# Optimization experiments

Hardware: AMD Instinct MI355X
Metric: run time of the kernel (lower is better)

The kernel has to match this reference:

```python
import jax, jax.numpy as jnp
import numpy as np

H, D = 4, 32
EMB = H * D  # 128
COUNTS = [30000, 20000, 25000, 50000]  # pesticide, disease, plant, event
EDGE_TYPES = [(0, 1), (1, 0), (2, 1), (1, 2), (3, 0), (0, 3), (3, 2), (2, 3)]
E = 200000
INV_SQRT_D = 1.0 / float(np.sqrt(D))


def layer_norm(x, g, b, eps=1e-5):
    m = x.mean(-1, keepdims=True)
    v = ((x - m) ** 2).mean(-1, keepdims=True)
    return (x - m) * jax.lax.rsqrt(v + eps) * g + b


def hgt_block(xs, edges, kqvW, kqvb, outW, outb, skip, a_rel, m_rel, p_rel, ln_g, ln_b):
    # type-specific K/Q/V projections -> [N, H, D]
    K, Q, V = [], [], []
    for t in range(4):
        kqv = jnp.einsum('nc,kdc->knd', xs[t], kqvW[t]) + kqvb[t][:, None, :]
        K.append(kqv[0].reshape(-1, H, D))
        Q.append(kqv[1].reshape(-1, H, D))
        V.append(kqv[2].reshape(-1, H, D))
    per_dst = {t: [] for t in range(4)}
    for r, (s, t) in enumerate(EDGE_TYPES):
        src, dst = edges[r, 0], edges[r, 1]
        k_rel = jnp.einsum('ehd,hdf->ehf', K[s][src], a_rel[r])  # relation-specific key transform
        v_rel = jnp.einsum('ehd,hdf->ehf', V[s][src], m_rel[r])  # relation-specific message transform
        logit = (k_rel * Q[t][dst]).sum(-1) * p_rel[r] * INV_SQRT_D  # [E, H]
        per_dst[t].append((logit, v_rel, dst))
    outs = []
    for t in range(4):
        N = xs[t].shape[0]
        logits = jnp.concatenate([p[0] for p in per_dst[t]], axis=0)
        vals = jnp.concatenate([p[1] for p in per_dst[t]], axis=0)
        idx = jnp.concatenate([p[2] for p in per_dst[t]], axis=0)
        # single segment softmax per destination node across ALL incoming edge types (PyG HGTConv)
        mx = jax.ops.segment_max(logits, idx, num_segments=N)
        ex = jnp.exp(logits - mx[idx])
        den = jax.ops.segment_sum(ex, idx, num_segments=N)
        alpha = ex / jnp.maximum(den[idx], 1e-16)
        agg = jax.ops.segment_sum(vals * alpha[..., None], idx, num_segments=N).reshape(N, EMB)
        o = jax.nn.gelu(agg, approximate=False) @ outW[t].T + outb[t]
        sg = jax.nn.sigmoid(skip[t])
        o = sg * o + (1.0 - sg) * xs[t]  # HGTConv learnable skip
        # HGTBlock: residual add, LayerNorm, ReLU (dropout = identity in eval)
        outs.append(jax.nn.relu(layer_norm(o + xs[t], ln_g, ln_b)))
    return outs


def fusion(seq, inW, inb, outW, outb, g, b):
    # seq: [N, 3, EMB]; torch MultiheadAttention self-attention, then mean + LN
    qkv = seq @ inW.T + inb  # [N, 3, 3*EMB]
    q, k, v = jnp.split(qkv, 3, axis=-1)
    heads = lambda x: x.reshape(x.shape[0], 3, H, D).transpose(0, 2, 1, 3)  # [N,H,3,D]
    q, k, v = heads(q), heads(k), heads(v)
    att = jax.nn.softmax(jnp.einsum('nhqd,nhkd->nhqk', q, k) * INV_SQRT_D, axis=-1)
    o = jnp.einsum('nhqk,nhkd->nhqd', att, v).transpose(0, 2, 1, 3).reshape(-1, 3, EMB)
    o = o @ outW.T + outb
    return layer_norm(o.mean(axis=1), g, b)


def _forward(x_pest, x_dis, x_plant, edges, proj_W, proj_b, event_emb, kqv_W, kqv_b,
             out_W, out_b, skip, a_rel, m_rel, p_rel, blk_ln_g, blk_ln_b,
             fin_W, fin_b, fout_W, fout_b, f_ln_g, f_ln_b):
    xs = [jax.nn.relu(x_pest @ proj_W[0].T + proj_b[0]),
          jax.nn.relu(x_dis @ proj_W[1].T + proj_b[1]),
          jax.nn.relu(x_plant @ proj_W[2].T + proj_b[2]),
          event_emb]  # event_emb(arange(N)) == the full table
    layers = []
    cur = xs
    for l in range(3):
        cur = hgt_block(cur, edges, kqv_W[l], kqv_b[l], out_W[l], out_b[l], skip[l],
                        a_rel[l], m_rel[l], p_rel[l], blk_ln_g[l], blk_ln_b[l])
        layers.append(cur)
    outs = []
    for j, t in enumerate([0, 1, 2]):  # pesticide, disease, plant
        seq = jnp.stack([layers[0][t], layers[1][t], layers[2][t]], axis=1)
        outs.append(fusion(seq, fin_W[j], fin_b[j], fout_W[j], fout_b[j], f_ln_g[j], f_ln_b[j]))
    return jnp.concatenate(outs, axis=0)  # [30000+20000+25000, 128]


def setup_inputs() -> dict:
    key = jax.random.key(0)
    ks = iter(jax.random.split(key, 64))
    nrm = lambda shape, s=0.05: jax.random.normal(next(ks), shape, dtype=jnp.float32) * s
    rows = []
    for s, t in EDGE_TYPES:
        rows.append(jnp.stack([jax.random.randint(next(ks), (E,), 0, COUNTS[s]),
                               jax.random.randint(next(ks), (E,), 0, COUNTS[t])]))
    return {
        'x_pest': nrm((COUNTS[0], 64), 1.0),
        'x_dis': nrm((COUNTS[1], 64), 1.0),
        'x_plant': nrm((COUNTS[2], 64), 1.0),
        'edges': jnp.stack(rows).astype(jnp.int32),  # [8, 2, E]
        'proj_W': nrm((3, EMB, 64)), 'proj_b': nrm((3, EMB)),
        'event_emb': nrm((COUNTS[3], EMB), 1.0),
        'kqv_W': nrm((3, 4, 3, EMB, EMB)), 'kqv_b': nrm((3, 4, 3, EMB)),
        'out_W': nrm((3, 4, EMB, EMB)), 'out_b': nrm((3, 4, EMB)),
        'skip': nrm((3, 4), 1.0),
        'a_rel': nrm((3, 8, H, D, D), 0.1), 'm_rel': nrm((3, 8, H, D, D), 0.1),
        'p_rel': jnp.ones((3, 8, H), jnp.float32),
        'blk_ln_g': jnp.ones((3, EMB), jnp.float32), 'blk_ln_b': jnp.zeros((3, EMB), jnp.float32),
        'fin_W': nrm((3, 3 * EMB, EMB)), 'fin_b': nrm((3, 3 * EMB)),
        'fout_W': nrm((3, EMB, EMB)), 'fout_b': nrm((3, EMB)),
        'f_ln_g': jnp.ones((3, EMB), jnp.float32), 'f_ln_b': jnp.zeros((3, EMB), jnp.float32),
    }


def reference(x_pest, x_dis, x_plant, edges, proj_W, proj_b, event_emb, kqv_W, kqv_b,
              out_W, out_b, skip, a_rel, m_rel, p_rel, blk_ln_g, blk_ln_b,
              fin_W, fin_b, fout_W, fout_b, f_ln_g, f_ln_b):
    return _forward(x_pest, x_dis, x_plant, edges, proj_W, proj_b, event_emb, kqv_W, kqv_b,
                    out_W, out_b, skip, a_rel, m_rel, p_rel, blk_ln_g, blk_ln_b,
                    fin_W, fin_b, fout_W, fout_b, f_ln_g, f_ln_b)
```

## Files before the change

kernel.cpp:

```cpp
#include <hip/hip_runtime.h>
#include <math.h>

#define E_CNT 200000
typedef unsigned short bfu;
typedef unsigned short u16;
typedef __attribute__((ext_vector_type(8))) short bh8;
typedef __attribute__((ext_vector_type(4))) float f4;

__device__ __forceinline__ float gelu_f(float x) {
    return 0.5f * x * (1.0f + erff(x * 0.70710678118654752f));
}
__device__ __forceinline__ float bf2f(bfu u) { return __uint_as_float(((unsigned)u) << 16); }
__device__ __forceinline__ bfu f2bf(float f) {
    unsigned u = __float_as_uint(f);
    unsigned r = u + 0x7FFFu + ((u >> 16) & 1u);
    return (bfu)(r >> 16);
}
__device__ __forceinline__ int rsrc_of(int r) {
    const int a[8] = {0, 1, 2, 1, 3, 0, 3, 2}; return a[r];
}
__device__ __forceinline__ int rdst_of(int r) {
    const int a[8] = {1, 0, 1, 2, 0, 3, 2, 3}; return a[r];
}
__device__ __forceinline__ int rpoff_of(int r) {
    const int a[9] = {0, 20001, 50002, 70003, 95004, 125005, 175006, 200007, 250008};
    return a[r];
}

__global__ __launch_bounds__(256) void fill_val(float* p, int n, float v) {
    int i = blockIdx.x * 256 + threadIdx.x;
    if (i < n) p[i] = v;
}

__global__ __launch_bounds__(256) void cvt_pack(
    const float* __restrict__ out_W, const float* __restrict__ kqv_W,
    const float* __restrict__ fin_W, const float* __restrict__ fout_W,
    const float* __restrict__ event_emb, const float* __restrict__ proj_W,
    bfu* __restrict__ OWB, bfu* __restrict__ KWB, bfu* __restrict__ FINWB,
    bfu* __restrict__ FOUTWB, bfu* __restrict__ EVB, bfu* __restrict__ PJWB)
{
    int i = blockIdx.x * 256 + threadIdx.x;
    const float* src; bfu* dst; size_t so, dox;
    if (i < 49152) { src = out_W; dst = OWB; so = (size_t)i * 4; dox = so; }
    else if (i < 98304) {
        int j = i - 49152; int m = j >> 12; int o = (j & 4095) * 4;
        src = kqv_W; dst = KWB;
        so = (size_t)m * 3 * 16384 + o; dox = (size_t)m * 16384 + o;
    }
    else if (i < 135168) { int j = i - 98304; src = fin_W; dst = FINWB; so = (size_t)j * 4; dox = so; }
    else if (i < 147456) { int j = i - 135168; src = fout_W; dst = FOUTWB; so = (size_t)j * 4; dox = so; }
    else if (i < 1747456) { int j = i - 147456; src = event_emb; dst = EVB; so = (size_t)j * 4; dox = so; }
    else if (i < 1753600) { int j = i - 1747456; src = proj_W; dst = PJWB; so = (size_t)j * 4; dox = so; }
    else return;
    float4 v = *(const float4*)(src + so);
    uint2 u;
    u.x = ((unsigned)f2bf(v.x)) | (((unsigned)f2bf(v.y)) << 16);
    u.y = ((unsigned)f2bf(v.z)) | (((unsigned)f2bf(v.w)) << 16);
    *(uint2*)(dst + dox) = u;
}

__global__ __launch_bounds__(256) void hist_all(const int* __restrict__ edges, int* __restrict__ rp) {
    int i = blockIdx.x * 256 + threadIdx.x;
    if (i >= 8 * E_CNT) return;
    int r = i / E_CNT, e = i - r * E_CNT;
    int d = edges[(size_t)(2 * r + 1) * E_CNT + e];
    atomicAdd(&rp[rpoff_of(r) + d + 1], 1);
}
__global__ __launch_bounds__(1024) void scan_part(int* __restrict__ a, int* __restrict__ part, int n) {
    __shared__ int lds[1024];
    int t = threadIdx.x, i = blockIdx.x * 1024 + t;
    int v = (i < n) ? a[i] : 0;
    lds[t] = v;
    __syncthreads();
    for (int off = 1; off < 1024; off <<= 1) {
        int u = (t >= off) ? lds[t - off] : 0;
        __syncthreads();
        lds[t] += u;
        __syncthreads();
    }
    if (i < n) a[i] = lds[t];
    if (t == 1023) part[blockIdx.x] = lds[1023];
}
__global__ __launch_bounds__(256) void scan_tot(int* __restrict__ part, int nb) {
    __shared__ int lds[256];
    int t = threadIdx.x;
    int v = (t < nb) ? part[t] : 0;
    lds[t] = v;
    __syncthreads();
    for (int off = 1; off < 256; off <<= 1) {
        int u = (t >= off) ? lds[t - off] : 0;
        __syncthreads();
        lds[t] += u;
        __syncthreads();
    }
    if (t < nb) part[t] = lds[t];
}
__global__ __launch_bounds__(1024) void scan_add(int* __restrict__ a, const int* __restrict__ part, int n) {
    int b = blockIdx.x + 1;
    int i = b * 1024 + threadIdx.x;
    if (i < n) a[i] += part[b - 1];
}
__global__ __launch_bounds__(256) void scatter_all(
    const int* __restrict__ edges, const int* __restrict__ RP,
    int* __restrict__ cur, u16* __restrict__ SIDX) {
    int i = blockIdx.x * 256 + threadIdx.x;
    if (i >= 8 * E_CNT) return;
    int r = i / E_CNT, e = i - r * E_CNT;
    int d = edges[(size_t)(2 * r + 1) * E_CNT + e];
    int pos = RP[rpoff_of(r) + d] + atomicAdd(&cur[r * 50000 + d], 1);
    SIDX[pos] = (u16)edges[(size_t)(2 * r) * E_CNT + e];
}

struct PDesc { const float* X; const bfu* W; const float* bias; bfu* Y; int N; int bend; };
struct PBatch { PDesc d[3]; };

__global__ __launch_bounds__(256) void mgemm_proj(PBatch pb) {
    int b = blockIdx.x;
    int gi = 0;
    #pragma unroll
    for (int k = 0; k < 2; ++k) gi += (b >= pb.d[k].bend) ? 1 : 0;
    const float* X = pb.d[0].X; const bfu* W = pb.d[0].W;
    const float* bi = pb.d[0].bias; bfu* Y = pb.d[0].Y;
    int N = pb.d[0].N, bstart = 0;
    #pragma unroll
    for (int k = 1; k < 3; ++k) {
        if (gi == k) {
            X = pb.d[k].X; W = pb.d[k].W; bi = pb.d[k].bias; Y = pb.d[k].Y;
            N = pb.d[k].N; bstart = pb.d[k - 1].bend;
        }
    }
    int bloc = b - bstart;
    const int tid = threadIdx.x;
    const int wave = tid >> 6, lane = tid & 63;
    const int row16 = lane & 15, kgrp = lane >> 4;
    const int r_base = bloc * 128 + wave * 32;
    f4 acc[2][8];
    #pragma unroll
    for (int t = 0; t < 2; ++t)
        #pragma unroll
        for (int n = 0; n < 8; ++n) acc[t][n] = (f4){0.f, 0.f, 0.f, 0.f};
    bh8 az = {0, 0, 0, 0, 0, 0, 0, 0};
    #pragma unroll
    for (int kb = 0; kb < 2; ++kb) {
        bh8 a[2] = {az, az};
        #pragma unroll
        for (int t = 0; t < 2; ++t) {
            int ar = r_base + t * 16 + row16;
            if (ar < N) {
                const float* xp = X + (size_t)ar * 64 + kb * 32 + kgrp * 8;
                float4 xa = *(const float4*)xp;
                float4 xb = *(const float4*)(xp + 4);
                a[t][0] = (short)f2bf(xa.x); a[t][1] = (short)f2bf(xa.y);
                a[t][2] = (short)f2bf(xa.z); a[t][3] = (short)f2bf(xa.w);
                a[t][4] = (short)f2bf(xb.x); a[t][5] = (short)f2bf(xb.y);
                a[t][6] = (short)f2bf(xb.z); a[t][7] = (short)f2bf(xb.w);
            }
        }
        #pragma unroll
        for (int n = 0; n < 8; ++n) {
            bh8 bv = *(const bh8*)(W + (size_t)(n * 16 + row16) * 64 + kb * 32 + kgrp * 8);
            acc[0][n] = __builtin_amdgcn_mfma_f32_16x16x32_bf16(a[0], bv, acc[0][n], 0, 0, 0);
            acc[1][n] = __builtin_amdgcn_mfma_f32_16x16x32_bf16(a[1], bv, acc[1][n], 0, 0, 0);
        }
    }
    #pragma unroll
    for (int t = 0; t < 2; ++t) {
        const int crow0 = r_base + t * 16 + kgrp * 4;
        #pragma unroll
        for (int n = 0; n < 8; ++n) {
            int col = n * 16 + row16;
            float bn = bi[col];
            #pragma unroll
            for (int j = 0; j < 4; ++j) {
                int row = crow0 + j;
                if (row < N) Y[(size_t)row * 128 + col] = f2bf(fmaxf(acc[t][n][j] + bn, 0.f));
            }
        }
    }
}

__global__ __launch_bounds__(256) void build_rel(
    const float* __restrict__ kqvW_l, const float* __restrict__ kqvb_l,
    const float* __restrict__ a_l, const float* __restrict__ m_l,
    bfu* __restrict__ WQAB, float* __restrict__ BQA,
    bfu* __restrict__ WVMB, float* __restrict__ BVM)
{
    __shared__ float As[32][33];
    __shared__ float Ws[32][129];
    int tid = threadIdx.x;
    int b = blockIdx.x;
    if (b < 32) {
        int r = b >> 2, h = b & 3;
        int dt = rdst_of(r);
        const float* Wq = kqvW_l + ((size_t)dt * 3 + 1) * 16384;
        const float* bq = kqvb_l + ((size_t)dt * 3 + 1) * 128;
        const float* A = a_l + (size_t)r * 4096 + h * 1024;
        for (int v = tid; v < 1024; v += 256) As[v >> 5][v & 31] = A[v];
        for (int v = tid; v < 4096; v += 256)
            Ws[v >> 7][v & 127] = Wq[(size_t)(h * 32 + (v >> 7)) * 128 + (v & 127)];
        __syncthreads();
        int c = tid & 127, half = tid >> 7;
        for (int d = half; d < 32; d += 2) {
            float acc = 0.f;
            #pragma unroll
            for (int f = 0; f < 32; ++f) acc = fmaf(As[d][f], Ws[f][c], acc);
            WQAB[((size_t)r * 128 + h * 32 + d) * 128 + c] = f2bf(acc);
        }
        if (tid < 32) {
            int d = tid;
            float acc = 0.f;
            #pragma unroll
            for (int f = 0; f < 32; ++f) acc = fmaf(As[d][f], bq[h * 32 + f], acc);
            BQA[(size_t)r * 128 + h * 32 + d] = acc;
        }
    } else {
        int bb2 = b - 32;
        int r = bb2 >> 2, h = bb2 & 3;
        int st = rsrc_of(r);
        const float* Wv = kqvW_l + ((size_t)st * 3 + 2) * 16384;
        const float* bv = kqvb_l + ((size_t)st * 3 + 2) * 128;
        const float* M = m_l + (size_t)r * 4096 + h * 1024;
        for (int v = tid; v < 1024; v += 256) As[v >> 5][v & 31] = M[v];
        for (int v = tid; v < 4096; v += 256)
            Ws[v >> 7][v & 127] = Wv[(size_t)(h * 32 + (v >> 7)) * 128 + (v & 127)];
        __syncthreads();
        int c = tid & 127, half = tid >> 7;
        for (int f = half; f < 32; f += 2) {
            float acc = 0.f;
            #pragma unroll
            for (int d = 0; d < 32; ++d) acc = fmaf(As[d][f], Ws[d][c], acc);
            WVMB[((size_t)r * 128 + h * 32 + f) * 128 + c] = f2bf(acc);
        }
        if (tid < 32) {
            int f = tid;
            float acc = 0.f;
            #pragma unroll
            for (int d = 0; d < 32; ++d) acc = fmaf(As[d][f], bv[h * 32 + d], acc);
            BVM[(size_t)r * 128 + h * 32 + f] = acc;
        }
    }
}

struct GDesc { const bfu* X; const bfu* W; const float* bias; bfu* Y; int N; int ldy; int bend; };
struct GBatch { GDesc d[9]; };

__global__ __launch_bounds__(256) void mgemm_batch(GBatch gb) {
    int b = blockIdx.x;
    int gi = 0;
    #pragma unroll
    for (int k = 0; k < 8; ++k) gi += (b >= gb.d[k].bend) ? 1 : 0;
    const bfu* X = gb.d[0].X; const bfu* W = gb.d[0].W;
    const float* bi = gb.d[0].bias; bfu* Y = gb.d[0].Y;
    int N = gb.d[0].N, ldy = gb.d[0].ldy, bstart = 0;
    #pragma unroll
    for (int k = 1; k < 9; ++k) {
        if (gi == k) {
            X = gb.d[k].X; W = gb.d[k].W; bi = gb.d[k].bias; Y = gb.d[k].Y;
            N = gb.d[k].N; ldy = gb.d[k].ldy; bstart = gb.d[k - 1].bend;
        }
    }
    int bloc = b - bstart;
    const int tid = threadIdx.x;
    const int wave = tid >> 6, lane = tid & 63;
    const int row16 = lane & 15, kgrp = lane >> 4;
    const int r_base = bloc * 128 + wave * 32;
    f4 acc[2][8];
    #pragma unroll
    for (int t = 0; t < 2; ++t)
        #pragma unroll
        for (int n = 0; n < 8; ++n) acc[t][n] = (f4){0.f, 0.f, 0.f, 0.f};
    bh8 az = {0, 0, 0, 0, 0, 0, 0, 0};
    #pragma unroll
    for (int kb = 0; kb < 4; ++kb) {
        int ar0 = r_base + row16, ar1 = r_base + 16 + row16;
        bh8 a0 = az, a1 = az;
        if (ar0 < N) a0 = *(const bh8*)(X + (size_t)ar0 * 128 + kb * 32 + kgrp * 8);
        if (ar1 < N) a1 = *(const bh8*)(X + (size_t)ar1 * 128 + kb * 32 + kgrp * 8);
        #pragma unroll
        for (int n = 0; n < 8; ++n) {
            bh8 bv = *(const bh8*)(W + (size_t)(n * 16 + row16) * 128 + kb * 32 + kgrp * 8);
            acc[0][n] = __builtin_amdgcn_mfma_f32_16x16x32_bf16(a0, bv, acc[0][n], 0, 0, 0);
            acc[1][n] = __builtin_amdgcn_mfma_f32_16x16x32_bf16(a1, bv, acc[1][n], 0, 0, 0);
        }
    }
    #pragma unroll
    for (int t = 0; t < 2; ++t) {
        const int crow0 = r_base + t * 16 + kgrp * 4;
        #pragma unroll
        for (int n = 0; n < 8; ++n) {
            int col = n * 16 + row16;
            float bn = bi[col];
            #pragma unroll
            for (int j = 0; j < 4; ++j) {
                int row = crow0 + j;
                if (row < N) Y[(size_t)row * ldy + col] = f2bf(acc[t][n][j] + bn);
            }
        }
    }
}

__global__ __launch_bounds__(256) void agg_dual(
    const bfu* QAA, const bfu* __restrict__ QAB,
    const bfu* __restrict__ KA, const bfu* __restrict__ VMA,
    const bfu* __restrict__ KB, const bfu* __restrict__ VMB,
    const int* __restrict__ rpA, const int* __restrict__ rpB,
    const u16* __restrict__ sidx,
    const float* __restrict__ prlA, const float* __restrict__ prlB,
    bfu* ACC, int Nn)
{
    int n = blockIdx.x * 4 + (threadIdx.x >> 6);
    if (n >= Nn) return;
    int l = threadIdx.x & 63;
    int h = l >> 4;
    const float scl = 0.17677669529663687f;

    float m = -3.0e38f, d = 0.f, a0 = 0.f, a1 = 0.f;

    auto upd = [&](float s, unsigned vu) {
        float nm = fmaxf(m, s);
        float sc = __expf(m - nm), w = __expf(s - nm);
        d = d * sc + w;
        a0 = fmaf(w, bf2f((bfu)vu), a0 * sc);
        a1 = fmaf(w, bf2f((bfu)(vu >> 16)), a1 * sc);
        m = nm;
    };

    auto rel = [&](const bfu* QA, const bfu* __restrict__ K, const bfu* __restrict__ VM,
                   const int* __restrict__ rp, const float* __restrict__ prl) {
        unsigned qu = *(const unsigned*)(QA + (size_t)n * 128 + 2 * l);
        float q0 = bf2f((bfu)qu), q1 = bf2f((bfu)(qu >> 16));
        float ph = prl[h] * scl;
        int i = rp[n], e1 = rp[n + 1];
        for (; i + 3 < e1; i += 4) {
            int sa = sidx[i], sb = sidx[i + 1], sc2 = sidx[i + 2], sd = sidx[i + 3];
            unsigned ka = *(const unsigned*)(K + (size_t)sa * 128 + 2 * l);
            unsigned kb = *(const unsigned*)(K + (size_t)sb * 128 + 2 * l);
            unsigned kc = *(const unsigned*)(K + (size_t)sc2 * 128 + 2 * l);
            unsigned kd = *(const unsigned*)(K + (size_t)sd * 128 + 2 * l);
            unsigned va = *(const unsigned*)(VM + (size_t)sa * 128 + 2 * l);
            unsigned vb = *(const unsigned*)(VM + (size_t)sb * 128 + 2 * l);
            unsigned vc = *(const unsigned*)(VM + (size_t)sc2 * 128 + 2 * l);
            unsigned vd = *(const unsigned*)(VM + (size_t)sd * 128 + 2 * l);
            float s0 = fmaf(bf2f((bfu)ka), q0, bf2f((bfu)(ka >> 16)) * q1);
            float s1 = fmaf(bf2f((bfu)kb), q0, bf2f((bfu)(kb >> 16)) * q1);
            float s2 = fmaf(bf2f((bfu)kc), q0, bf2f((bfu)(kc >> 16)) * q1);
            float s3 = fmaf(bf2f((bfu)kd), q0, bf2f((bfu)(kd >> 16)) * q1);
            #pragma unroll
            for (int off = 1; off <= 8; off <<= 1) {
                s0 += __shfl_xor(s0, off);
                s1 += __shfl_xor(s1, off);
                s2 += __shfl_xor(s2, off);
                s3 += __shfl_xor(s3, off);
            }
            upd(s0 * ph, va);
            upd(s1 * ph, vb);
            upd(s2 * ph, vc);
            upd(s3 * ph, vd);
        }
        for (; i < e1; ++i) {
            int sa = sidx[i];
            unsigned ka = *(const unsigned*)(K + (size_t)sa * 128 + 2 * l);
            unsigned va = *(const unsigned*)(VM + (size_t)sa * 128 + 2 * l);
            float s0 = fmaf(bf2f((bfu)ka), q0, bf2f((bfu)(ka >> 16)) * q1);
            #pragma unroll
            for (int off = 1; off <= 8; off <<= 1) s0 += __shfl_xor(s0, off);
            upd(s0 * ph, va);
        }
    };
    rel(QAA, KA, VMA, rpA, prlA);
    rel(QAB, KB, VMB, rpB, prlB);

    float rd = 1.f / fmaxf(d, 1e-16f);
    float y0 = gelu_f(a0 * rd);
    float y1 = gelu_f(a1 * rd);
    unsigned ou = ((unsigned)f2bf(y0)) | (((unsigned)f2bf(y1)) << 16);
    *(unsigned*)(ACC + (size_t)n * 128 + 2 * l) = ou;
}

__global__ __launch_bounds__(256) void mgemm_epi_layer(
    const bfu* __restrict__ A, const bfu* __restrict__ W, const float* __restrict__ bias,
    const bfu* __restrict__ Xr, const float* __restrict__ skp,
    const float* __restrict__ g, const float* __restrict__ bb,
    bfu* __restrict__ Y, int N)
{
    const int tid = threadIdx.x;
    const int wave = tid >> 6, lane = tid & 63;
    const int row16 = lane & 15, kgrp = lane >> 4;
    const int r_base = blockIdx.x * 64 + wave * 16;
    const int arow = r_base + row16;
    f4 acc[8];
    #pragma unroll
    for (int n = 0; n < 8; ++n) acc[n] = (f4){0.f, 0.f, 0.f, 0.f};
    bh8 az = {0, 0, 0, 0, 0, 0, 0, 0};
    #pragma unroll
    for (int kb = 0; kb < 4; ++kb) {
        bh8 a = az;
        if (arow < N) a = *(const bh8*)(A + (size_t)arow * 128 + kb * 32 + kgrp * 8);
        #pragma unroll
        for (int n = 0; n < 8; ++n) {
            bh8 bv = *(const bh8*)(W + (size_t)(n * 16 + row16) * 128 + kb * 32 + kgrp * 8);
            acc[n] = __builtin_amdgcn_mfma_f32_16x16x32_bf16(a, bv, acc[n], 0, 0, 0);
        }
    }
    const int crow0 = r_base + kgrp * 4;
    float sg = 1.f / (1.f + expf(-skp[0]));
    float z[8][4];
    #pragma unroll
    for (int n = 0; n < 8; ++n) {
        float bn = bias[n * 16 + row16];
        #pragma unroll
        for (int j = 0; j < 4; ++j) z[n][j] = acc[n][j] + bn;
    }
    #pragma unroll
    for (int j = 0; j < 4; ++j) {
        int row = crow0 + j;
        if (row >= N) continue;
        #pragma unroll
        for (int n = 0; n < 8; ++n) {
            float xr = bf2f(Xr[(size_t)row * 128 + n * 16 + row16]);
            z[n][j] = sg * z[n][j] + (1.f - sg) * xr + xr;
        }
    }
    float s[4], q[4];
    #pragma unroll
    for (int j = 0; j < 4; ++j) {
        s[j] = 0.f; q[j] = 0.f;
        #pragma unroll
        for (int n = 0; n < 8; ++n) { s[j] += z[n][j]; q[j] += z[n][j] * z[n][j]; }
    }
    #pragma unroll
    for (int off = 1; off <= 8; off <<= 1) {
        #pragma unroll
        for (int j = 0; j < 4; ++j) {
            s[j] += __shfl_xor(s[j], off);
            q[j] += __shfl_xor(q[j], off);
        }
    }
    #pragma unroll
    for (int j = 0; j < 4; ++j) {
        int row = crow0 + j;
        if (row >= N) continue;
        float mean = s[j] * (1.f / 128.f);
        float var = q[j] * (1.f / 128.f) - mean * mean;
        float inv = rsqrtf(var + 1e-5f);
        #pragma unroll
        for (int n = 0; n < 8; ++n) {
            int col = n * 16 + row16;
            float y = (z[n][j] - mean) * inv * g[col] + bb[col];
            Y[(size_t)row * 128 + col] = f2bf(fmaxf(y, 0.f));
        }
    }
}

__global__ __launch_bounds__(256) void mgemm_epi_ln(
    const bfu* __restrict__ X, const bfu* __restrict__ W, const float* __restrict__ bias,
    const float* __restrict__ g, const float* __restrict__ bb,
    float* __restrict__ Y, int N)
{
    const int tid = threadIdx.x;
    const int wave = tid >> 6, lane = tid & 63;
    const int row16 = lane & 15, kgrp = lane >> 4;
    const int r_base = blockIdx.x * 64 + wave * 16;
    const int arow = r_base + row16;
    f4 acc[8];
    #pragma unroll
    for (int n = 0; n < 8; ++n) acc[n] = (f4){0.f, 0.f, 0.f, 0.f};
    bh8 az = {0, 0, 0, 0, 0, 0, 0, 0};
    #pragma unroll
    for (int kb = 0; kb < 4; ++kb) {
        bh8 a = az;
        if (arow < N) a = *(const bh8*)(X + (size_t)arow * 128 + kb * 32 + kgrp * 8);
        #pragma unroll
        for (int n = 0; n < 8; ++n) {
            bh8 bv = *(const bh8*)(W + (size_t)(n * 16 + row16) * 128 + kb * 32 + kgrp * 8);
            acc[n] = __builtin_amdgcn_mfma_f32_16x16x32_bf16(a, bv, acc[n], 0, 0, 0);
        }
    }
    const int crow0 = r_base + kgrp * 4;
    float z[8][4];
    #pragma unroll
    for (int n = 0; n < 8; ++n) {
        float bn = bias[n * 16 + row16];
        #pragma unroll
        for (int j = 0; j < 4; ++j) z[n][j] = acc[n][j] + bn;
    }
    float s[4], q[4];
    #pragma unroll
    for (int j = 0; j < 4; ++j) {
        s[j] = 0.f; q[j] = 0.f;
        #pragma unroll
        for (int n = 0; n < 8; ++n) { s[j] += z[n][j]; q[j] += z[n][j] * z[n][j]; }
    }
    #pragma unroll
    for (int off = 1; off <= 8; off <<= 1) {
        #pragma unroll
        for (int j = 0; j < 4; ++j) {
            s[j] += __shfl_xor(s[j], off);
            q[j] += __shfl_xor(q[j], off);
        }
    }
    #pragma unroll
    for (int j = 0; j < 4; ++j) {
        int row = crow0 + j;
        if (row >= N) continue;
        float mean = s[j] * (1.f / 128.f);
        float var = q[j] * (1.f / 128.f) - mean * mean;
        float inv = rsqrtf(var + 1e-5f);
        #pragma unroll
        for (int n = 0; n < 8; ++n) {
            int col = n * 16 + row16;
            Y[(size_t)row * 128 + col] = (z[n][j] - mean) * inv * g[col] + bb[col];
        }
    }
}

__global__ __launch_bounds__(256) void attn_fuse(
    const bfu* __restrict__ QKV, bfu* __restrict__ OM, int M)
{
    int n = blockIdx.x * 4 + (threadIdx.x >> 6);
    int l = threadIdx.x & 63;
    if (n >= M) return;
    const bfu* base = QKV + (size_t)n * 1152;
    float q[3][2], k[3][2], v[3][2];
    #pragma unroll
    for (int p = 0; p < 3; ++p) {
        q[p][0] = bf2f(base[(0 * 3 + p) * 128 + l]);
        q[p][1] = bf2f(base[(0 * 3 + p) * 128 + l + 64]);
        k[p][0] = bf2f(base[(1 * 3 + p) * 128 + l]);
        k[p][1] = bf2f(base[(1 * 3 + p) * 128 + l + 64]);
        v[p][0] = bf2f(base[(2 * 3 + p) * 128 + l]);
        v[p][1] = bf2f(base[(2 * 3 + p) * 128 + l + 64]);
    }
    float lgA[3][3], lgB[3][3];
    #pragma unroll
    for (int qi = 0; qi < 3; ++qi)
        #pragma unroll
        for (int ki = 0; ki < 3; ++ki) {
            float s0 = q[qi][0] * k[ki][0];
            float s1 = q[qi][1] * k[ki][1];
            #pragma unroll
            for (int off = 1; off <= 16; off <<= 1) {
                s0 += __shfl_xor(s0, off);
                s1 += __shfl_xor(s1, off);
            }
            lgA[qi][ki] = s0 * 0.17677669529663687f;
            lgB[qi][ki] = s1 * 0.17677669529663687f;
        }
    float oA = 0.f, oB = 0.f;
    #pragma unroll
    for (int qi = 0; qi < 3; ++qi) {
        float mA = fmaxf(lgA[qi][0], fmaxf(lgA[qi][1], lgA[qi][2]));
        float e0 = __expf(lgA[qi][0] - mA), e1 = __expf(lgA[qi][1] - mA), e2 = __expf(lgA[qi][2] - mA);
        float rd = 1.f / (e0 + e1 + e2);
        oA += (e0 * v[0][0] + e1 * v[1][0] + e2 * v[2][0]) * rd;
        float mB = fmaxf(lgB[qi][0], fmaxf(lgB[qi][1], lgB[qi][2]));
        float f0 = __expf(lgB[qi][0] - mB), f1 = __expf(lgB[qi][1] - mB), f2 = __expf(lgB[qi][2] - mB);
        float rdB = 1.f / (f0 + f1 + f2);
        oB += (f0 * v[0][1] + f1 * v[1][1] + f2 * v[2][1]) * rdB;
    }
    OM[(size_t)n * 128 + l] = f2bf(oA * (1.f / 3.f));
    OM[(size_t)n * 128 + l + 64] = f2bf(oB * (1.f / 3.f));
}

extern "C" void kernel_launch(void* const* d_in, const int* in_sizes, int n_in,
                              void* d_out, int out_size, void* d_ws, size_t ws_size,
                              hipStream_t stream)
{
    const float* x_pest   = (const float*)d_in[0];
    const float* x_dis    = (const float*)d_in[1];
    const float* x_plant  = (const float*)d_in[2];
    const int*   edges    = (const int*)d_in[3];
    const float* proj_W   = (const float*)d_in[4];
    const float* proj_b   = (const float*)d_in[5];
    const float* event_emb= (const float*)d_in[6];
    const float* kqv_W    = (const float*)d_in[7];
    const float* kqv_b    = (const float*)d_in[8];
    const float* out_W    = (const float*)d_in[9];
    const float* out_b    = (const float*)d_in[10];
    const float* skip     = (const float*)d_in[11];
    const float* a_rel    = (const float*)d_in[12];
    const float* m_rel    = (const float*)d_in[13];
    const float* p_rel    = (const float*)d_in[14];
    const float* blk_ln_g = (const float*)d_in[15];
    const float* blk_ln_b = (const float*)d_in[16];
    const float* fin_W    = (const float*)d_in[17];
    const float* fin_b    = (const float*)d_in[18];
    const float* fout_W   = (const float*)d_in[19];
    const float* fout_b   = (const float*)d_in[20];
    const float* f_ln_g   = (const float*)d_in[21];
    const float* f_ln_b   = (const float*)d_in[22];
    float* out = (float*)d_out;

    static const int NT[4]  = {30000, 20000, 25000, 50000};
    static const int OFF[4] = {0, 30000, 50000, 75000};
    static const int RPOFF[9] = {0, 20001, 50002, 70003, 95004, 125005, 175006, 200007, 250008};
    static const int DG[4][2][2] = { {{1,1},{4,3}}, {{0,0},{2,2}}, {{3,1},{6,3}}, {{5,0},{7,2}} };

    char* wsb = (char*)d_ws;
    size_t ob = 0;
    auto alc = [&](size_t bytes) -> void* {
        void* p = wsb + ob; ob += (bytes + 255) & ~(size_t)255; return p;
    };
    bfu* LK0  = (bfu*)alc((size_t)75000 * 128 * 2);
    bfu* LK1  = (bfu*)alc((size_t)75000 * 128 * 2);
    bfu* POOL = (bfu*)alc((size_t)210000 * 128 * 2);
    bfu* WQAB = (bfu*)alc((size_t)8 * 16384 * 2);
    float* BQA = (float*)alc((size_t)8 * 128 * 4);
    bfu* WVMB = (bfu*)alc((size_t)8 * 16384 * 2);
    float* BVM = (float*)alc((size_t)8 * 128 * 4);
    bfu* KWB  = (bfu*)alc((size_t)12 * 16384 * 2);
    bfu* OWB  = (bfu*)alc((size_t)12 * 16384 * 2);
    bfu* FINWB = (bfu*)alc((size_t)3 * 49152 * 2);
    bfu* FOUTWB = (bfu*)alc((size_t)3 * 16384 * 2);
    bfu* PJWB = (bfu*)alc((size_t)3 * 8192 * 2);
    int* RP   = (int*)alc((size_t)250008 * 4);
    int* PART = (int*)alc(1024);
    u16* SIDX = (u16*)alc((size_t)8 * E_CNT * 2);
    if (ws_size < ob) {
        fill_val<<<(out_size + 255) / 256, 256, 0, stream>>>(out, out_size, 1e30f);
        return;
    }
    int* CUR = (int*)POOL;
    bfu* QKVf = POOL;
    bfu* OMB  = POOL + (size_t)20000 * 1152;

    bfu* EVB = (bfu*)out;
    bfu* XB  = (bfu*)((char*)out + 12800000);
    bfu* L2F = (bfu*)((char*)out + 19200000);

    cvt_pack<<<(1753600 + 255) / 256, 256, 0, stream>>>(
        out_W, kqv_W, fin_W, fout_W, event_emb, proj_W,
        OWB, KWB, FINWB, FOUTWB, EVB, PJWB);

    hipMemsetAsync(RP, 0, (size_t)250008 * 4, stream);
    const int eg8 = (8 * E_CNT + 255) / 256;
    hist_all<<<eg8, 256, 0, stream>>>(edges, RP);
    scan_part<<<245, 1024, 0, stream>>>(RP, PART, 250008);
    scan_tot<<<1, 256, 0, stream>>>(PART, 245);
    scan_add<<<244, 1024, 0, stream>>>(RP, PART, 250008);
    hipMemsetAsync(CUR, 0, (size_t)8 * 50000 * 4, stream);
    scatter_all<<<eg8, 256, 0, stream>>>(edges, RP, CUR, SIDX);

    {
        PBatch pb;
        const float* xin0[3] = {x_pest, x_dis, x_plant};
        int acc = 0;
        for (int t = 0; t < 3; ++t) {
            pb.d[t].X = xin0[t];
            pb.d[t].W = PJWB + (size_t)t * 8192;
            pb.d[t].bias = proj_b + (size_t)t * 128;
            pb.d[t].Y = XB + (size_t)OFF[t] * 128;
            pb.d[t].N = NT[t];
            acc += (NT[t] + 127) / 128;
            pb.d[t].bend = acc;
        }
        mgemm_proj<<<acc, 256, 0, stream>>>(pb);
    }

    auto launch_batch = [&](GDesc* ds, int cnt) {
        GBatch gb;
        int acc = 0;
        for (int i = 0; i < cnt; ++i) {
            gb.d[i] = ds[i];
            acc += (ds[i].N + 127) / 128;
            gb.d[i].bend = acc;
        }
        for (int i = cnt; i < 9; ++i) { gb.d[i] = gb.d[cnt - 1]; gb.d[i].bend = acc; }
        mgemm_batch<<<acc, 256, 0, stream>>>(gb);
    };

    for (int l = 0; l < 3; ++l) {
        const float* kqvW_l = kqv_W + (size_t)l * 12 * 16384;
        const float* kqvb_l = kqv_b + (size_t)l * 12 * 128;
        build_rel<<<64, 256, 0, stream>>>(kqvW_l, kqvb_l,
            a_rel + (size_t)l * 8 * 4096, m_rel + (size_t)l * 8 * 4096,
            WQAB, BQA, WVMB, BVM);

        auto feat_ptr = [&](int tt) -> const bfu* {
            if (tt == 3) return EVB;
            if (l == 0) return XB + (size_t)OFF[tt] * 128;
            return (l == 1 ? LK0 : LK1) + (size_t)OFF[tt] * 128;
        };

        int nord = (l == 2) ? 3 : 4;
        for (int dt = 0; dt < nord; ++dt) {
            int Ndt = NT[dt];
            int rA = DG[dt][0][0], sA = DG[dt][0][1];
            int rB = DG[dt][1][0], sB = DG[dt][1][1];
            int NsA = NT[sA], NsB = NT[sB];
            bfu* QA_A = POOL;
            bfu* QA_B = QA_A + (size_t)Ndt * 128;
            bfu* K_A  = QA_B + (size_t)Ndt * 128;
            bfu* VM_A = K_A + (size_t)NsA * 128;
            bfu* K_B  = VM_A + (size_t)NsA * 128;
            bfu* VM_B = K_B + (size_t)NsB * 128;

            GDesc ds[6];
            ds[0] = { feat_ptr(dt), WQAB + (size_t)rA * 16384, BQA + (size_t)rA * 128, QA_A, Ndt, 128, 0 };
            ds[1] = { feat_ptr(dt), WQAB + (size_t)rB * 16384, BQA + (size_t)rB * 128, QA_B, Ndt, 128, 0 };
            ds[2] = { feat_ptr(sA), KWB + (size_t)(l * 4 + sA) * 16384,
                      kqvb_l + ((size_t)sA * 3 + 0) * 128, K_A, NsA, 128, 0 };
            ds[3] = { feat_ptr(sA), WVMB + (size_t)rA * 16384, BVM + (size_t)rA * 128, VM_A, NsA, 128, 0 };
            ds[4] = { feat_ptr(sB), KWB + (size_t)(l * 4 + sB) * 16384,
                      kqvb_l + ((size_t)sB * 3 + 0) * 128, K_B, NsB, 128, 0 };
            ds[5] = { feat_ptr(sB), WVMB + (size_t)rB * 16384, BVM + (size_t)rB * 128, VM_B, NsB, 128, 0 };
            launch_batch(ds, 6);

            agg_dual<<<(Ndt + 3) / 4, 256, 0, stream>>>(
                QA_A, QA_B, K_A, VM_A, K_B, VM_B,
                RP + RPOFF[rA], RP + RPOFF[rB], SIDX,
                p_rel + (size_t)(l * 8 + rA) * 4, p_rel + (size_t)(l * 8 + rB) * 4,
                QA_A , Ndt);

            size_t wi = (size_t)l * 4 + dt;
            const bfu* xr = feat_ptr(dt);
            bfu* ydst = (dt == 3) ? EVB :
                        (l == 0 ? LK0 : (l == 1 ? LK1 : L2F)) + (size_t)OFF[dt] * 128;
            mgemm_epi_layer<<<(Ndt + 63) / 64, 256, 0, stream>>>(
                QA_A, OWB + wi * 16384, out_b + wi * 128, xr, skip + wi,
                blk_ln_g + (size_t)l * 128, blk_ln_b + (size_t)l * 128, ydst, Ndt);
        }
    }

    const int CH = 20000;
    for (int j = 0; j < 3; ++j) {
        int Nj = NT[j];
        for (int b0 = 0; b0 < Nj; b0 += CH) {
            int M = min(CH, Nj - b0);
            const bfu* srcs[3] = {
                LK0 + (size_t)(OFF[j] + b0) * 128,
                LK1 + (size_t)(OFF[j] + b0) * 128,
                L2F + (size_t)(OFF[j] + b0) * 128 };
            GDesc ds[9];
            int di = 0;
            for (int kk = 0; kk < 3; ++kk)
                for (int p = 0; p < 3; ++p) {
                    ds[di++] = { srcs[p], FINWB + (size_t)j * 49152 + (size_t)kk * 16384,
                                 fin_b + (size_t)j * 384 + kk * 128,
                                 QKVf + (size_t)(kk * 3 + p) * 128, M, 1152, 0 };
                }
            launch_batch(ds, 9);
            attn_fuse<<<(M + 3) / 4, 256, 0, stream>>>(QKVf, OMB, M);
            mgemm_epi_ln<<<(M + 63) / 64, 256, 0, stream>>>(
                OMB, FOUTWB + (size_t)j * 16384, fout_b + (size_t)j * 128,
                f_ln_g + (size_t)j * 128, f_ln_b + (size_t)j * 128,
                out + (size_t)(OFF[j] + b0) * 128, M);
        }
    }
}
```

Baseline: 1.702 ms.

## Interleave K and V rows and split online softmax into two chains

The projection GEMMs now write K and the relation-transformed V into one interleaved buffer with a 256-element row stride, so each gathered source node's K and V sit in the same 512-byte span. This is meant to improve locality of the random gathers in the aggregation kernel. The online-softmax state is split into two independent accumulators that alternate across unrolled edges and are merged at the end. That shortens the serial dependency chain of exp/fma updates, at the cost of extra registers and a final merge step.

```diff
diff --git a/kernel.cpp b/kernel.cpp
--- a/kernel.cpp
+++ b/kernel.cpp
@@ -301,8 +301,7 @@
 
 __global__ __launch_bounds__(256) void agg_dual(
     const bfu* QAA, const bfu* __restrict__ QAB,
-    const bfu* __restrict__ KA, const bfu* __restrict__ VMA,
-    const bfu* __restrict__ KB, const bfu* __restrict__ VMB,
+    const bfu* __restrict__ KVA, const bfu* __restrict__ KVB,
     const int* __restrict__ rpA, const int* __restrict__ rpB,
     const u16* __restrict__ sidx,
     const float* __restrict__ prlA, const float* __restrict__ prlB,
@@ -314,18 +313,27 @@
     int h = l >> 4;
     const float scl = 0.17677669529663687f;
 
-    float m = -3.0e38f, d = 0.f, a0 = 0.f, a1 = 0.f;
-
-    auto upd = [&](float s, unsigned vu) {
-        float nm = fmaxf(m, s);
-        float sc = __expf(m - nm), w = __expf(s - nm);
-        d = d * sc + w;
-        a0 = fmaf(w, bf2f((bfu)vu), a0 * sc);
-        a1 = fmaf(w, bf2f((bfu)(vu >> 16)), a1 * sc);
-        m = nm;
+    float m0 = -3.0e38f, d0 = 0.f, x0 = 0.f, y0 = 0.f;
+    float m1 = -3.0e38f, d1 = 0.f, x1 = 0.f, y1 = 0.f;
+
+    auto upd0 = [&](float s, unsigned vu) {
+        float nm = fmaxf(m0, s);
+        float sc = __expf(m0 - nm), w = __expf(s - nm);
+        d0 = d0 * sc + w;
+        x0 = fmaf(w, bf2f((bfu)vu), x0 * sc);
+        y0 = fmaf(w, bf2f((bfu)(vu >> 16)), y0 * sc);
+        m0 = nm;
     };
-
-    auto rel = [&](const bfu* QA, const bfu* __restrict__ K, const bfu* __restrict__ VM,
+    auto upd1 = [&](float s, unsigned vu) {
+        float nm = fmaxf(m1, s);
+        float sc = __expf(m1 - nm), w = __expf(s - nm);
+        d1 = d1 * sc + w;
+        x1 = fmaf(w, bf2f((bfu)vu), x1 * sc);
+        y1 = fmaf(w, bf2f((bfu)(vu >> 16)), y1 * sc);
+        m1 = nm;
+    };
+
+    auto rel = [&](const bfu* QA, const bfu* __restrict__ KV,
                    const int* __restrict__ rp, const float* __restrict__ prl) {
         unsigned qu = *(const unsigned*)(QA + (size_t)n * 128 + 2 * l);
         float q0 = bf2f((bfu)qu), q1 = bf2f((bfu)(qu >> 16));
@@ -333,14 +341,18 @@
         int i = rp[n], e1 = rp[n + 1];
         for (; i + 3 < e1; i += 4) {
             int sa = sidx[i], sb = sidx[i + 1], sc2 = sidx[i + 2], sd = sidx[i + 3];
-            unsigned ka = *(const unsigned*)(K + (size_t)sa * 128 + 2 * l);
-            unsigned kb = *(const unsigned*)(K + (size_t)sb * 128 + 2 * l);
-            unsigned kc = *(const unsigned*)(K + (size_t)sc2 * 128 + 2 * l);
-            unsigned kd = *(const unsigned*)(K + (size_t)sd * 128 + 2 * l);
-            unsigned va = *(const unsigned*)(VM + (size_t)sa * 128 + 2 * l);
-            unsigned vb = *(const unsigned*)(VM + (size_t)sb * 128 + 2 * l);
-            unsigned vc = *(const unsigned*)(VM + (size_t)sc2 * 128 + 2 * l);
-            unsigned vd = *(const unsigned*)(VM + (size_t)sd * 128 + 2 * l);
+            const bfu* pa = KV + (size_t)sa * 256 + 2 * l;
+            const bfu* pb = KV + (size_t)sb * 256 + 2 * l;
+            const bfu* pc = KV + (size_t)sc2 * 256 + 2 * l;
+            const bfu* pd = KV + (size_t)sd * 256 + 2 * l;
+            unsigned ka = *(const unsigned*)pa;
+            unsigned kb = *(const unsigned*)pb;
+            unsigned kc = *(const unsigned*)pc;
+            unsigned kd = *(const unsigned*)pd;
+            unsigned va = *(const unsigned*)(pa + 128);
+            unsigned vb = *(const unsigned*)(pb + 128);
+            unsigned vc = *(const unsigned*)(pc + 128);
+            unsigned vd = *(const unsigned*)(pd + 128);
             float s0 = fmaf(bf2f((bfu)ka), q0, bf2f((bfu)(ka >> 16)) * q1);
             float s1 = fmaf(bf2f((bfu)kb), q0, bf2f((bfu)(kb >> 16)) * q1);
             float s2 = fmaf(bf2f((bfu)kc), q0, bf2f((bfu)(kc >> 16)) * q1);
@@ -352,28 +364,35 @@
                 s2 += __shfl_xor(s2, off);
                 s3 += __shfl_xor(s3, off);
             }
-            upd(s0 * ph, va);
-            upd(s1 * ph, vb);
-            upd(s2 * ph, vc);
-            upd(s3 * ph, vd);
+            upd0(s0 * ph, va);
+            upd1(s1 * ph, vb);
+            upd0(s2 * ph, vc);
+            upd1(s3 * ph, vd);
         }
         for (; i < e1; ++i) {
             int sa = sidx[i];
-            unsigned ka = *(const unsigned*)(K + (size_t)sa * 128 + 2 * l);
-            unsigned va = *(const unsigned*)(VM + (size_t)sa * 128 + 2 * l);
+            const bfu* pa = KV + (size_t)sa * 256 + 2 * l;
+            unsigned ka = *(const unsigned*)pa;
+            unsigned va = *(const unsigned*)(pa + 128);
             float s0 = fmaf(bf2f((bfu)ka), q0, bf2f((bfu)(ka >> 16)) * q1);
             #pragma unroll
             for (int off = 1; off <= 8; off <<= 1) s0 += __shfl_xor(s0, off);
-            upd(s0 * ph, va);
+            upd0(s0 * ph, va);
         }
     };
-    rel(QAA, KA, VMA, rpA, prlA);
-    rel(QAB, KB, VMB, rpB, prlB);
+    rel(QAA, KVA, rpA, prlA);
+    rel(QAB, KVB, rpB, prlB);
+
+    float nm = fmaxf(m0, m1);
+    float sA = __expf(m0 - nm), sB = __expf(m1 - nm);
+    float d = d0 * sA + d1 * sB;
+    float a0 = x0 * sA + x1 * sB;
+    float a1 = y0 * sA + y1 * sB;
 
     float rd = 1.f / fmaxf(d, 1e-16f);
-    float y0 = gelu_f(a0 * rd);
-    float y1 = gelu_f(a1 * rd);
-    unsigned ou = ((unsigned)f2bf(y0)) | (((unsigned)f2bf(y1)) << 16);
+    float o0 = gelu_f(a0 * rd);
+    float o1 = gelu_f(a1 * rd);
+    unsigned ou = ((unsigned)f2bf(o0)) | (((unsigned)f2bf(o1)) << 16);
     *(unsigned*)(ACC + (size_t)n * 128 + 2 * l) = ou;
 }
 
@@ -690,24 +709,22 @@
             int NsA = NT[sA], NsB = NT[sB];
             bfu* QA_A = POOL;
             bfu* QA_B = QA_A + (size_t)Ndt * 128;
-            bfu* K_A  = QA_B + (size_t)Ndt * 128;
-            bfu* VM_A = K_A + (size_t)NsA * 128;
-            bfu* K_B  = VM_A + (size_t)NsA * 128;
-            bfu* VM_B = K_B + (size_t)NsB * 128;
+            bfu* KV_A = QA_B + (size_t)Ndt * 128;
+            bfu* KV_B = KV_A + (size_t)NsA * 256;
 
             GDesc ds[6];
             ds[0] = { feat_ptr(dt), WQAB + (size_t)rA * 16384, BQA + (size_t)rA * 128, QA_A, Ndt, 128, 0 };
             ds[1] = { feat_ptr(dt), WQAB + (size_t)rB * 16384, BQA + (size_t)rB * 128, QA_B, Ndt, 128, 0 };
             ds[2] = { feat_ptr(sA), KWB + (size_t)(l * 4 + sA) * 16384,
-                      kqvb_l + ((size_t)sA * 3 + 0) * 128, K_A, NsA, 128, 0 };
-            ds[3] = { feat_ptr(sA), WVMB + (size_t)rA * 16384, BVM + (size_t)rA * 128, VM_A, NsA, 128, 0 };
+                      kqvb_l + ((size_t)sA * 3 + 0) * 128, KV_A, NsA, 256, 0 };
+            ds[3] = { feat_ptr(sA), WVMB + (size_t)rA * 16384, BVM + (size_t)rA * 128, KV_A + 128, NsA, 256, 0 };
             ds[4] = { feat_ptr(sB), KWB + (size_t)(l * 4 + sB) * 16384,
-                      kqvb_l + ((size_t)sB * 3 + 0) * 128, K_B, NsB, 128, 0 };
-            ds[5] = { feat_ptr(sB), WVMB + (size_t)rB * 16384, BVM + (size_t)rB * 128, VM_B, NsB, 128, 0 };
+                      kqvb_l + ((size_t)sB * 3 + 0) * 128, KV_B, NsB, 256, 0 };
+            ds[5] = { feat_ptr(sB), WVMB + (size_t)rB * 16384, BVM + (size_t)rB * 128, KV_B + 128, NsB, 256, 0 };
             launch_batch(ds, 6);
 
             agg_dual<<<(Ndt + 3) / 4, 256, 0, stream>>>(
-                QA_A, QA_B, K_A, VM_A, K_B, VM_B,
+                QA_A, QA_B, KV_A, KV_B,
                 RP + RPOFF[rA], RP + RPOFF[rB], SIDX,
                 p_rel + (size_t)(l * 8 + rA) * 4, p_rel + (size_t)(l * 8 + rB) * 4,
                 QA_A , Ndt);
```

Measured after the change: 1.697 ms. Within noise of the previous version (-0.3%).
